# Optimization experiments

Measured on AMD Instinct MI355X. Metric: run time of the kernel, lower is better.

## Reference

```python
import jax, jax.numpy as jnp
import numpy as np
from jax import lax


def setup_inputs() -> dict:
    key = jax.random.key(0)
    k1, k2, k3, k4 = jax.random.split(key, 4)
    N, T = 4096, 64          # num_nodes, tokens per node
    V, H, L = 30000, 256, 2  # vocab, hidden size, LSTM layers
    data = jax.random.randint(k1, (N, T), 0, V, dtype=jnp.int64)
    embed = jax.random.uniform(k2, (V, H), jnp.float32, -0.1, 0.1)
    Wx = jax.random.normal(k3, (L, H, 4 * H), jnp.float32) * 0.05
    Wh = jax.random.normal(k4, (L, H, 4 * H), jnp.float32) * 0.05
    b = jnp.zeros((L, 4 * H), jnp.float32)
    return {"data": data, "embed": embed, "Wx": Wx, "Wh": Wh, "b": b}


def _stacked_lstm_last(tok, Wx, Wh, b):
    # tok: [N, T, H]; Wx/Wh: [L, H, 4H]; b: [L, 4H]
    L, H = Wx.shape[0], Wx.shape[1]
    N = tok.shape[0]
    xs = jnp.swapaxes(tok, 0, 1)  # [T, N, H] -- scan over time, batched over nodes
    c0 = jnp.zeros((L, N, H), tok.dtype)
    h0 = jnp.zeros((L, N, H), tok.dtype)

    def step(carry, x_t):
        c, h = carry
        inp = x_t
        new_c, new_h = [], []
        for l in range(L):  # small fixed layer loop
            z = inp @ Wx[l] + h[l] @ Wh[l] + b[l]  # [N, 4H]
            i, f, g, o = jnp.split(z, 4, axis=-1)   # flax gate order i, f, g, o
            i, f, o = jax.nn.sigmoid(i), jax.nn.sigmoid(f), jax.nn.sigmoid(o)
            g = jnp.tanh(g)
            cl = f * c[l] + i * g
            hl = o * jnp.tanh(cl)
            new_c.append(cl)
            new_h.append(hl)
            inp = hl  # top layer output feeds next layer
        return (jnp.stack(new_c), jnp.stack(new_h)), None

    (_, hF), _ = lax.scan(step, (c0, h0), xs)
    # result[-1] in the original is the top-layer output at the final step,
    # which equals the final top-layer hidden state.
    return hF[-1]  # [N, H]


def reference(data, embed, Wx, Wh, b):
    tok = embed[data]  # [N, T, H] embedding lookup
    return _stacked_lstm_last(tok, Wx, Wh, b)
```

## Files before the change

kernel.cpp:

```cpp
#include <hip/hip_runtime.h>
#include <hip/hip_bf16.h>

#define TT 64
#define HH 256
#define GG 1024

typedef _Float16 f16;
typedef __attribute__((ext_vector_type(8))) _Float16 f16x8;
typedef __attribute__((ext_vector_type(4))) _Float16 f16x4;
typedef __attribute__((ext_vector_type(4))) float f32x4;

__device__ __forceinline__ float exp2_(float x) { return __builtin_amdgcn_exp2f(x); }
__device__ __forceinline__ float sig_(float x) {
    return __builtin_amdgcn_rcpf(1.0f + exp2_(-1.44269504f * x));
}
__device__ __forceinline__ float tanh_(float x) {
    return 1.0f - 2.0f * __builtin_amdgcn_rcpf(1.0f + exp2_(2.88539008f * x));
}
__device__ __forceinline__ float sigp_(float x) { return 1.0f / (1.0f + __expf(-x)); }
__device__ __forceinline__ float tanhp_(float x) {
    x = fminf(fmaxf(x, -15.0f), 15.0f);
    float e = __expf(-2.0f * x);
    return (1.0f - e) / (1.0f + e);
}

__global__ void pack_weights(const float* __restrict__ Wx, const float* __restrict__ Wh,
                             f16* __restrict__ Wp) {
    int t = blockIdx.x * 256 + threadIdx.x;
    int lane = t & 63;
    int nt = (t >> 6) & 63;
    int kk = (t >> 12) & 15;
    int l = t >> 16;
    int n = nt * 16 + (lane & 15);
    int kbase = kk * 32 + 8 * (lane >> 4);
    const float* src = (kbase < 256) ? (Wx + (size_t)l * HH * GG + (size_t)kbase * GG + n)
                                     : (Wh + (size_t)l * HH * GG + (size_t)(kbase - 256) * GG + n);
    f16x8 v;
#pragma unroll
    for (int j = 0; j < 8; ++j) v[j] = (f16)src[(size_t)j * GG];
    *(f16x8*)(Wp + (size_t)t * 8) = v;
}

__global__ __launch_bounds__(512) void embw_gemm(
    const float* __restrict__ embed, const float* __restrict__ bias,
    const f16* __restrict__ Wp, f16* __restrict__ embW, int vocab)
{
    __shared__ f16 a_lds[32 * HH];
    const int tid = threadIdx.x;
    const int lane = tid & 63;
    const int w = tid >> 6;
    const int arow = lane & 15;
    const int g4 = lane >> 4;
    const int r0 = blockIdx.x * 32;

#pragma unroll
    for (int i = 0; i < 4; ++i) {
        int chunk = tid + i * 512;
        int row = chunk >> 6;
        int c4 = chunk & 63;
        int grow = r0 + row; if (grow >= vocab) grow = vocab - 1;
        float4 v = *(const float4*)(embed + (size_t)grow * HH + c4 * 4);
        int idx = row * HH + ((c4 * 4) ^ ((row & 7) << 3));
        *(f16x4*)&a_lds[idx] = (f16x4){(f16)v.x, (f16)v.y, (f16)v.z, (f16)v.w};
    }
    __syncthreads();

    float breg[8];
#pragma unroll
    for (int tt = 0; tt < 8; ++tt) breg[tt] = bias[(w * 8 + tt) * 16 + arow];

    f32x4 acc[2][8];
#pragma unroll
    for (int mt = 0; mt < 2; ++mt)
#pragma unroll
        for (int tt = 0; tt < 8; ++tt)
            acc[mt][tt] = (f32x4){breg[tt], breg[tt], breg[tt], breg[tt]};

    const f16* wl = Wp + (size_t)lane * 8;
#pragma unroll 2
    for (int kk = 0; kk < 8; ++kk) {
        int sw = (kk * 32 + g4 * 8) ^ ((arow & 7) << 3);
        f16x8 a0 = *(const f16x8*)&a_lds[arow * HH + sw];
        f16x8 a1 = *(const f16x8*)&a_lds[(arow + 16) * HH + sw];
        const f16* wkk = wl + (size_t)kk * 64 * 64 * 8;
#pragma unroll
        for (int tt = 0; tt < 8; ++tt) {
            f16x8 b = *(const f16x8*)(wkk + (size_t)(w * 8 + tt) * 64 * 8);
            acc[0][tt] = __builtin_amdgcn_mfma_f32_16x16x32_f16(a0, b, acc[0][tt], 0, 0, 0);
            acc[1][tt] = __builtin_amdgcn_mfma_f32_16x16x32_f16(a1, b, acc[1][tt], 0, 0, 0);
        }
    }

#pragma unroll
    for (int mt = 0; mt < 2; ++mt)
#pragma unroll
        for (int tt = 0; tt < 8; ++tt)
#pragma unroll
            for (int r = 0; r < 4; ++r) {
                int row = r0 + mt * 16 + g4 * 4 + r;
                if (row < vocab) {
                    int col = (w * 8 + tt) * 16 + arow;
                    embW[(size_t)row * GG + col] = (f16)acc[mt][tt][r];
                }
            }
}

#define NB2 32
#define LDZ 1032
#define LDH 264

__global__ __launch_bounds__(512, 1) void lstm_rec2(
    const int* __restrict__ data, const float* __restrict__ bias,
    const f16* __restrict__ embW, const f16* __restrict__ Wp,
    float* __restrict__ out)
{
    __shared__ f16 zx[NB2 * LDZ];
    __shared__ f16 h0s[NB2 * LDH];
    __shared__ f16 h1s[NB2 * LDH];

    const int tid = threadIdx.x;
    const int lane = tid & 63;
    const int w = tid >> 6;
    const int arow = lane & 15;
    const int g4 = lane >> 4;
    const int n0 = blockIdx.x * NB2;

    const int sn = tid >> 4;
    const int scg = (tid & 15) * 64;
    const int srow_base = (n0 + sn) * TT;

    for (int i = tid; i < NB2 * LDH; i += 512) { h0s[i] = (f16)0; h1s[i] = (f16)0; }

    float breg1[8];
#pragma unroll
    for (int tt = 0; tt < 8; ++tt) {
        int col = (tt >> 1) * 256 + w * 32 + (tt & 1) * 16 + arow;
        breg1[tt] = bias[GG + col];
    }

    float c0[16], c1[16];
#pragma unroll
    for (int i = 0; i < 16; ++i) { c0[i] = 0.0f; c1[i] = 0.0f; }

    const f16* wl0 = Wp + (size_t)8 * 64 * 64 * 8 + (size_t)lane * 8;
    const f16* wl1 = Wp + (size_t)16 * 64 * 64 * 8 + (size_t)lane * 8;

#pragma unroll 1
    for (int t = 0; t < TT; ++t) {
        {
            int row = data[srow_base + t];
            const f16* src = embW + (size_t)row * GG + scg;
            f16* dst = &zx[sn * LDZ + scg];
#pragma unroll
            for (int j = 0; j < 8; ++j)
                *(f16x8*)(dst + j * 8) = *(const f16x8*)(src + j * 8);
        }
        __syncthreads();

        f32x4 acc[2][8];
#pragma unroll
        for (int mt = 0; mt < 2; ++mt)
#pragma unroll
            for (int tt = 0; tt < 8; ++tt) {
                int col = (tt >> 1) * 256 + w * 32 + (tt & 1) * 16 + arow;
#pragma unroll
                for (int r = 0; r < 4; ++r)
                    acc[mt][tt][r] = (float)zx[(mt * 16 + g4 * 4 + r) * LDZ + col];
            }

#pragma unroll 2
        for (int kk = 0; kk < 8; ++kk) {
            int k0 = kk * 32 + 8 * g4;
            f16x8 a0 = *(const f16x8*)&h0s[arow * LDH + k0];
            f16x8 a1 = *(const f16x8*)&h0s[(arow + 16) * LDH + k0];
            const f16* wkk = wl0 + (size_t)kk * 64 * 64 * 8;
#pragma unroll
            for (int tt = 0; tt < 8; ++tt) {
                int nt = (tt >> 1) * 16 + w * 2 + (tt & 1);
                f16x8 b = *(const f16x8*)(wkk + (size_t)nt * 64 * 8);
                acc[0][tt] = __builtin_amdgcn_mfma_f32_16x16x32_f16(a0, b, acc[0][tt], 0, 0, 0);
                acc[1][tt] = __builtin_amdgcn_mfma_f32_16x16x32_f16(a1, b, acc[1][tt], 0, 0, 0);
            }
        }
        __syncthreads();

#pragma unroll
        for (int mt = 0; mt < 2; ++mt)
#pragma unroll
            for (int sub = 0; sub < 2; ++sub)
#pragma unroll
                for (int r = 0; r < 4; ++r) {
                    int node = mt * 16 + g4 * 4 + r;
                    float i_ = sig_(acc[mt][0 + sub][r]);
                    float f_ = sig_(acc[mt][2 + sub][r]);
                    float g_ = tanh_(acc[mt][4 + sub][r]);
                    float o_ = sig_(acc[mt][6 + sub][r]);
                    int ci = mt * 8 + sub * 4 + r;
                    float c = fmaf(f_, c0[ci], i_ * g_);
                    c0[ci] = c;
                    int u = w * 32 + sub * 16 + arow;
                    h0s[node * LDH + u] = (f16)(o_ * tanh_(c));
                }
        __syncthreads();

        f32x4 acc1[2][8];
#pragma unroll
        for (int mt = 0; mt < 2; ++mt)
#pragma unroll
            for (int tt = 0; tt < 8; ++tt)
                acc1[mt][tt] = (f32x4){breg1[tt], breg1[tt], breg1[tt], breg1[tt]};

#pragma unroll 2
        for (int kk = 0; kk < 16; ++kk) {
            const f16* asrc = (kk < 8) ? h0s : h1s;
            int k0 = (kk & 7) * 32 + 8 * g4;
            f16x8 a0 = *(const f16x8*)&asrc[arow * LDH + k0];
            f16x8 a1 = *(const f16x8*)&asrc[(arow + 16) * LDH + k0];
            const f16* wkk = wl1 + (size_t)kk * 64 * 64 * 8;
#pragma unroll
            for (int tt = 0; tt < 8; ++tt) {
                int nt = (tt >> 1) * 16 + w * 2 + (tt & 1);
                f16x8 b = *(const f16x8*)(wkk + (size_t)nt * 64 * 8);
                acc1[0][tt] = __builtin_amdgcn_mfma_f32_16x16x32_f16(a0, b, acc1[0][tt], 0, 0, 0);
                acc1[1][tt] = __builtin_amdgcn_mfma_f32_16x16x32_f16(a1, b, acc1[1][tt], 0, 0, 0);
            }
        }
        __syncthreads();

#pragma unroll
        for (int mt = 0; mt < 2; ++mt)
#pragma unroll
            for (int sub = 0; sub < 2; ++sub)
#pragma unroll
                for (int r = 0; r < 4; ++r) {
                    int node = mt * 16 + g4 * 4 + r;
                    float i_ = sig_(acc1[mt][0 + sub][r]);
                    float f_ = sig_(acc1[mt][2 + sub][r]);
                    float g_ = tanh_(acc1[mt][4 + sub][r]);
                    float o_ = sig_(acc1[mt][6 + sub][r]);
                    int ci = mt * 8 + sub * 4 + r;
                    float c = fmaf(f_, c1[ci], i_ * g_);
                    c1[ci] = c;
                    int u = w * 32 + sub * 16 + arow;
                    h1s[node * LDH + u] = (f16)(o_ * tanh_(c));
                }
    }
    __syncthreads();

    for (int i = tid; i < NB2 * HH; i += 512) {
        int n = i >> 8, k = i & 255;
        out[(size_t)(n0 + n) * HH + k] = (float)h1s[n * LDH + k];
    }
}

__global__ void convert_embed(const float* __restrict__ e, f16* __restrict__ o, int n8) {
    int i = blockIdx.x * 256 + threadIdx.x;
    if (i >= n8) return;
    size_t p = (size_t)i * 8;
    float4 a = *(const float4*)(e + p);
    float4 b = *(const float4*)(e + p + 4);
    f16x8 v = { (f16)a.x, (f16)a.y, (f16)a.z, (f16)a.w,
                (f16)b.x, (f16)b.y, (f16)b.z, (f16)b.w };
    *(f16x8*)(o + p) = v;
}

#define FB 32
#define FTH 512
#define FLD 264
__device__ __forceinline__ void fb_layer_step(
    const f16 (*bx)[FLD], f16 (*bh)[FLD], const f16* __restrict__ wlayer,
    const float* breg_l, float* c_l, int lane, int w)
{
    f32x4 acc[2][8];
#pragma unroll
    for (int mt = 0; mt < 2; ++mt)
#pragma unroll
        for (int tt = 0; tt < 8; ++tt) {
            float b = breg_l[tt];
            acc[mt][tt] = (f32x4){b, b, b, b};
        }
    const int arow = lane & 15;
    const int koff = 8 * (lane >> 4);
    const f16* wl = wlayer + (size_t)lane * 8;
#pragma unroll 2
    for (int kk = 0; kk < 16; ++kk) {
        int k0 = (kk & 7) * 32 + koff;
        const f16(*src)[FLD] = (kk < 8) ? bx : (const f16(*)[FLD])bh;
        f16x8 a0 = *(const f16x8*)&src[arow][k0];
        f16x8 a1 = *(const f16x8*)&src[arow + 16][k0];
        const f16* wkk = wl + (size_t)kk * 64 * 64 * 8;
#pragma unroll
        for (int tt = 0; tt < 8; ++tt) {
            int nt = (tt >> 1) * 16 + w * 2 + (tt & 1);
            f16x8 b = *(const f16x8*)(wkk + (size_t)nt * 64 * 8);
            acc[0][tt] = __builtin_amdgcn_mfma_f32_16x16x32_f16(a0, b, acc[0][tt], 0, 0, 0);
            acc[1][tt] = __builtin_amdgcn_mfma_f32_16x16x32_f16(a1, b, acc[1][tt], 0, 0, 0);
        }
    }
    __syncthreads();
#pragma unroll
    for (int mt = 0; mt < 2; ++mt)
#pragma unroll
        for (int sub = 0; sub < 2; ++sub) {
            f32x4 iv = acc[mt][0 + sub], fv = acc[mt][2 + sub];
            f32x4 gv = acc[mt][4 + sub], ov = acc[mt][6 + sub];
#pragma unroll
            for (int r = 0; r < 4; ++r) {
                float i_ = sigp_(iv[r]), f_ = sigp_(fv[r]), g_ = tanhp_(gv[r]), o_ = sigp_(ov[r]);
                int ci = mt * 8 + sub * 4 + r;
                float c = fmaf(f_, c_l[ci], i_ * g_);
                c_l[ci] = c;
                int node = mt * 16 + (lane >> 4) * 4 + r;
                int unit = w * 32 + sub * 16 + (lane & 15);
                bh[node][unit] = (f16)(o_ * tanhp_(c));
            }
        }
    __syncthreads();
}

__global__ __launch_bounds__(FTH, 2) void lstm_mfma_fb(
    const int* __restrict__ data, const float* __restrict__ bias,
    const f16* __restrict__ emb, const f16* __restrict__ Wp,
    float* __restrict__ out, int vocab)
{
    __shared__ f16 x_lds[FB][FLD];
    __shared__ f16 h0_lds[FB][FLD];
    __shared__ f16 h1_lds[FB][FLD];
    const int tid = threadIdx.x;
    const int lane = tid & 63;
    const int w = tid >> 6;
    const int n0 = blockIdx.x * FB;
    for (int i = tid; i < FB * FLD; i += FTH) {
        (&h0_lds[0][0])[i] = (f16)0.0f; (&h1_lds[0][0])[i] = (f16)0.0f;
    }
    float breg[2][8];
#pragma unroll
    for (int l = 0; l < 2; ++l)
#pragma unroll
        for (int tt = 0; tt < 8; ++tt) {
            int col = (tt >> 1) * 256 + w * 32 + (tt & 1) * 16 + (lane & 15);
            breg[l][tt] = bias[l * GG + col];
        }
    float cst[2][16];
#pragma unroll
    for (int i = 0; i < 32; ++i) (&cst[0][0])[i] = 0.0f;
    __syncthreads();
    const f16* Wp0 = Wp;
    const f16* Wp1 = Wp + (size_t)16 * 64 * 64 * 8;
    for (int t = 0; t < TT; ++t) {
        {
            int n = tid >> 4;
            int cg = (tid & 15) * 16;
            int row = data[(n0 + n) * TT + t];
            row = min(max(row, 0), vocab - 1);
            const f16* src = emb + (size_t)row * HH + cg;
            *(f16x8*)&x_lds[n][cg] = *(const f16x8*)src;
            *(f16x8*)&x_lds[n][cg + 8] = *(const f16x8*)(src + 8);
        }
        __syncthreads();
        fb_layer_step(x_lds, h0_lds, Wp0, breg[0], cst[0], lane, w);
        fb_layer_step((const f16(*)[FLD])h0_lds, h1_lds, Wp1, breg[1], cst[1], lane, w);
    }
    for (int i = tid; i < FB * HH; i += FTH) {
        int n = i >> 8, k = i & 255;
        out[(size_t)(n0 + n) * HH + k] = (float)h1_lds[n][k];
    }
}

extern "C" void kernel_launch(void* const* d_in, const int* in_sizes, int n_in,
                              void* d_out, int out_size, void* d_ws, size_t ws_size,
                              hipStream_t stream) {
    const int* data = (const int*)d_in[0];
    const float* embed = (const float*)d_in[1];
    const float* Wx = (const float*)d_in[2];
    const float* Wh = (const float*)d_in[3];
    const float* bias = (const float*)d_in[4];
    float* out = (float*)d_out;
    const int vocab = in_sizes[1] / HH;
    const int nNodes = in_sizes[0] / TT;

    const size_t wp_bytes = (size_t)2 * 16 * 64 * 64 * 8 * 2;
    const size_t embw_bytes = (size_t)vocab * GG * 2;
    const size_t emb16_bytes = (size_t)vocab * HH * 2;

    if (ws_size >= embw_bytes + wp_bytes) {
        f16* embW = (f16*)d_ws;
        f16* Wp = (f16*)((char*)d_ws + embw_bytes);
        pack_weights<<<dim3(512), dim3(256), 0, stream>>>(Wx, Wh, Wp);
        embw_gemm<<<dim3((vocab + 31) / 32), dim3(512), 0, stream>>>(embed, bias, Wp, embW, vocab);
        lstm_rec2<<<dim3(nNodes / NB2), dim3(512), 0, stream>>>(data, bias, embW, Wp, out);
        return;
    }
    f16* emb_h = (f16*)d_ws;
    f16* Wp = (f16*)((char*)d_ws + emb16_bytes);
    int n8 = in_sizes[1] / 8;
    convert_embed<<<dim3((n8 + 255) / 256), dim3(256), 0, stream>>>(embed, emb_h, n8);
    pack_weights<<<dim3(512), dim3(256), 0, stream>>>(Wx, Wh, Wp);
    lstm_mfma_fb<<<dim3(nNodes / FB), dim3(FTH), 0, stream>>>(data, bias, emb_h, Wp, out, vocab);
}
```

Measured before the change: 1.228 ms.

## Permute precomputed embedding-gate layout so each lane loads its gate inputs directly

The precompute kernel now writes the embedding-times-Wx table in a permuted column order, so each lane's eight gate columns for one row are contiguous. The recurrent kernel drops the per-step LDS staging of gathered rows and its barrier. Instead, each lane issues four 16-byte global loads straight into its accumulator registers, using token ids preloaded into LDS once at kernel start. This removes an LDS round trip and a __syncthreads per timestep, at the cost of scattered global gathers sitting on the critical path of each step.

```diff
diff --git a/kernel.cpp b/kernel.cpp
--- a/kernel.cpp
+++ b/kernel.cpp
@@ -94,19 +94,20 @@
 #pragma unroll
     for (int mt = 0; mt < 2; ++mt)
 #pragma unroll
-        for (int tt = 0; tt < 8; ++tt)
+        for (int tt = 0; tt < 8; ++tt) {
+            int nt = w * 8 + tt;
+            int cw = (nt >> 1) & 7;
+            int ctt = ((nt >> 4) << 1) | (nt & 1);
 #pragma unroll
             for (int r = 0; r < 4; ++r) {
                 int row = r0 + mt * 16 + g4 * 4 + r;
-                if (row < vocab) {
-                    int col = (w * 8 + tt) * 16 + arow;
-                    embW[(size_t)row * GG + col] = (f16)acc[mt][tt][r];
-                }
-            }
+                if (row < vocab)
+                    embW[(size_t)row * GG + cw * 128 + arow * 8 + ctt] = (f16)acc[mt][tt][r];
+            }
+        }
 }
 
 #define NB2 32
-#define LDZ 1032
 #define LDH 264
 
 __global__ __launch_bounds__(512, 1) void lstm_rec2(
@@ -114,9 +115,9 @@
     const f16* __restrict__ embW, const f16* __restrict__ Wp,
     float* __restrict__ out)
 {
-    __shared__ f16 zx[NB2 * LDZ];
     __shared__ f16 h0s[NB2 * LDH];
     __shared__ f16 h1s[NB2 * LDH];
+    __shared__ int toks[NB2 * TT];
 
     const int tid = threadIdx.x;
     const int lane = tid & 63;
@@ -125,11 +126,8 @@
     const int g4 = lane >> 4;
     const int n0 = blockIdx.x * NB2;
 
-    const int sn = tid >> 4;
-    const int scg = (tid & 15) * 64;
-    const int srow_base = (n0 + sn) * TT;
-
     for (int i = tid; i < NB2 * LDH; i += 512) { h0s[i] = (f16)0; h1s[i] = (f16)0; }
+    for (int i = tid; i < NB2 * TT; i += 512) toks[i] = data[n0 * TT + i];
 
     float breg1[8];
 #pragma unroll
@@ -144,29 +142,35 @@
 
     const f16* wl0 = Wp + (size_t)8 * 64 * 64 * 8 + (size_t)lane * 8;
     const f16* wl1 = Wp + (size_t)16 * 64 * 64 * 8 + (size_t)lane * 8;
+    const int zoff = w * 128 + arow * 8;
+
+    __syncthreads();
 
 #pragma unroll 1
     for (int t = 0; t < TT; ++t) {
-        {
-            int row = data[srow_base + t];
-            const f16* src = embW + (size_t)row * GG + scg;
-            f16* dst = &zx[sn * LDZ + scg];
-#pragma unroll
-            for (int j = 0; j < 8; ++j)
-                *(f16x8*)(dst + j * 8) = *(const f16x8*)(src + j * 8);
-        }
-        __syncthreads();
-
         f32x4 acc[2][8];
 #pragma unroll
-        for (int mt = 0; mt < 2; ++mt)
+        for (int mt = 0; mt < 2; ++mt) {
+            f16x8 zf0, zf1, zf2, zf3;
+            {
+                int nb = mt * 16 + g4 * 4;
+                int t0 = toks[(nb + 0) * TT + t];
+                int t1 = toks[(nb + 1) * TT + t];
+                int t2 = toks[(nb + 2) * TT + t];
+                int t3 = toks[(nb + 3) * TT + t];
+                zf0 = *(const f16x8*)(embW + (size_t)t0 * GG + zoff);
+                zf1 = *(const f16x8*)(embW + (size_t)t1 * GG + zoff);
+                zf2 = *(const f16x8*)(embW + (size_t)t2 * GG + zoff);
+                zf3 = *(const f16x8*)(embW + (size_t)t3 * GG + zoff);
+            }
 #pragma unroll
             for (int tt = 0; tt < 8; ++tt) {
-                int col = (tt >> 1) * 256 + w * 32 + (tt & 1) * 16 + arow;
-#pragma unroll
-                for (int r = 0; r < 4; ++r)
-                    acc[mt][tt][r] = (float)zx[(mt * 16 + g4 * 4 + r) * LDZ + col];
-            }
+                acc[mt][tt][0] = (float)zf0[tt];
+                acc[mt][tt][1] = (float)zf1[tt];
+                acc[mt][tt][2] = (float)zf2[tt];
+                acc[mt][tt][3] = (float)zf3[tt];
+            }
+        }
 
 #pragma unroll 2
         for (int kk = 0; kk < 8; ++kk) {
```

Result: slower. 1.324 ms (+7.8%).
